# Kernel optimization log

Measured on AMD Instinct MI355X. Metric: run time of the kernel, lower is better.

Reference implementation:

```python
import jax, jax.numpy as jnp
import numpy as np

N_NODES = 50000
N_EDGES = 1600000
IN_DIM = 1024
HID = 2048
OUT = 3
BN_EPS = 1e-5


def _degree_norms(src, dst):
    ones = jnp.ones((src.shape[0],), jnp.float32)
    out_deg = jax.ops.segment_sum(ones, src, num_segments=N_NODES)
    in_deg = jax.ops.segment_sum(ones, dst, num_segments=N_NODES)
    # DGL GraphConv norm='both' clamps degrees to min 1
    out_norm = jnp.clip(out_deg, 1.0) ** -0.5
    in_norm = jnp.clip(in_deg, 1.0) ** -0.5
    return out_norm, in_norm


def _graph_conv(h, src, dst, out_norm, in_norm, W, b):
    # symmetric-normalized SpMM aggregate then dense transform (DGL GraphConv, norm='both')
    h = h * out_norm[:, None]
    msg = h[src]                                   # [E, F] gather
    agg = jax.ops.segment_sum(msg, dst, num_segments=N_NODES)
    agg = agg * in_norm[:, None]
    return agg @ W + b


def setup_inputs() -> dict:
    key = jax.random.key(0)
    k1, k2, k3, k4, k5, k6, k7 = jax.random.split(key, 7)
    in_feat = jax.random.normal(k1, (N_NODES, IN_DIM), jnp.float32)
    src = jax.random.randint(k2, (N_EDGES,), 0, N_NODES, jnp.int32)
    dst = jax.random.randint(k3, (N_EDGES,), 0, N_NODES, jnp.int32)
    W1 = jax.random.normal(k4, (IN_DIM, HID), jnp.float32) * (1.0 / np.sqrt(IN_DIM))
    b1 = jnp.zeros((HID,), jnp.float32)
    Wout = jax.random.normal(k5, (HID, OUT), jnp.float32) * (1.0 / np.sqrt(HID))
    bout = jnp.zeros((OUT,), jnp.float32)
    return {"in_feat": in_feat, "src": src, "dst": dst,
            "W1": W1, "b1": b1, "Wout": Wout, "bout": bout}


def reference(in_feat, src, dst, W1, b1, Wout, bout):
    out_norm, in_norm = _degree_norms(src, dst)
    h = _graph_conv(in_feat, src, dst, out_norm, in_norm, W1, b1)
    h = jax.nn.relu(h)
    # freshly-instantiated BatchNorm1d in training mode: batch stats, gamma=1, beta=0
    mean = jnp.mean(h, axis=0, keepdims=True)
    var = jnp.var(h, axis=0, keepdims=True)
    h = (h - mean) * jax.lax.rsqrt(var + BN_EPS)
    h = _graph_conv(h, src, dst, out_norm, in_norm, Wout, bout)
    return jax.nn.softmax(h, axis=1)
```

## Files before the change

kernel.cpp:

```cpp
#include <hip/hip_runtime.h>
#include <hip/hip_bf16.h>
#include <stdint.h>

#define N_NODES 50000
#define N_EDGES 1600000
#define IN_DIM  1024
#define HID     2048
#define OUTC    3
#define M_PAD   50048
#define BN_EPS  1e-5f

#define SCAN_CH 512
#define NCH     98

#define NPAN    32
#define PF      32
#define PSTRIDE ((size_t)M_PAD * PF)
#define NGRP    782
#define NXCD    8
#define DUMMY_SRC N_NODES
#define E_PAD_MAX (N_EDGES + 3 * N_NODES)

typedef __bf16 bf16_t;
typedef __bf16 bf16x4_t __attribute__((ext_vector_type(4)));
typedef __bf16 bf16x8_t __attribute__((ext_vector_type(8)));
typedef float  f32x4_t  __attribute__((ext_vector_type(4)));

__device__ __forceinline__ void gl2lds16(const void* g, void* l) {
  __builtin_amdgcn_global_load_lds((const __attribute__((address_space(1))) uint32_t*)g,
                                   (__attribute__((address_space(3))) uint32_t*)l,
                                   16, 0, 0);
}

__global__ void k_hist(const int* __restrict__ src, const int* __restrict__ dst,
                       int* out_cnt, int* in_cnt) {
  int e = blockIdx.x * 256 + threadIdx.x;
  if (e < N_EDGES) {
    atomicAdd(&out_cnt[src[e]], 1);
    atomicAdd(&in_cnt[dst[e]], 1);
  }
}

__global__ void k_norms(const int* __restrict__ out_cnt, const int* __restrict__ in_cnt,
                        float* out_norm, float* in_norm) {
  int i = blockIdx.x * 256 + threadIdx.x;
  if (i < N_NODES) {
    out_norm[i] = rsqrtf((float)max(out_cnt[i], 1));
    in_norm[i]  = rsqrtf((float)max(in_cnt[i], 1));
  }
}

__global__ void k_scan1(const int* __restrict__ deg, int* incl, int* partial) {
  __shared__ int s[SCAN_CH];
  int tid = threadIdx.x;
  int i = blockIdx.x * SCAN_CH + tid;
  int v = (i < N_NODES) ? ((deg[i] + 3) & ~3) : 0;
  s[tid] = v;
  for (int off = 1; off < SCAN_CH; off <<= 1) {
    __syncthreads();
    int x = (tid >= off) ? s[tid - off] : 0;
    __syncthreads();
    s[tid] += x;
  }
  __syncthreads();
  if (i < N_NODES) incl[i] = s[tid];
  if (tid == SCAN_CH - 1) partial[blockIdx.x] = s[tid];
}

__global__ void k_scan2(const int* __restrict__ partial, int* chunk_off, int* row_ptr) {
  if (threadIdx.x == 0 && blockIdx.x == 0) {
    int run = 0;
    for (int b = 0; b < NCH; b++) { chunk_off[b] = run; run += partial[b]; }
    row_ptr[N_NODES] = run;
  }
}

__global__ void k_scan3(const int* __restrict__ deg, const int* __restrict__ incl,
                        const int* __restrict__ chunk_off, int* row_ptr, int* cursor) {
  int i = blockIdx.x * SCAN_CH + threadIdx.x;
  if (i < N_NODES) {
    int dp = (deg[i] + 3) & ~3;
    int e = chunk_off[blockIdx.x] + incl[i] - dp;
    row_ptr[i] = e;
    cursor[i]  = e;
  }
}

__global__ void k_fill(const int* __restrict__ src, const int* __restrict__ dst,
                       int* cursor, int* csr_src) {
  int e = blockIdx.x * 256 + threadIdx.x;
  if (e < N_EDGES) {
    int p = atomicAdd(&cursor[dst[e]], 1);
    csr_src[p] = src[e];
  }
}

__global__ void k_pad(const int* __restrict__ in_cnt, const int* __restrict__ row_ptr,
                      int* csr_src) {
  int i = blockIdx.x * 256 + threadIdx.x;
  if (i < N_NODES) {
    int d = in_cnt[i], dp = (d + 3) & ~3;
    int base = row_ptr[i];
    for (int j = d; j < dp; j++) csr_src[base + j] = DUMMY_SRC;
  }
}

__global__ void k_conv(const float* __restrict__ in_feat, const float* __restrict__ out_norm,
                       bf16_t* __restrict__ xbp) {
  int node = blockIdx.x, t = threadIdx.x;
  int p = t >> 3, fo = (t & 7) * 4;
  bf16x4_t o;
  if (node < N_NODES) {
    float on = out_norm[node];
    float4 v = *(const float4*)(in_feat + (size_t)node * IN_DIM + p * PF + fo);
    o[0] = (bf16_t)(v.x * on); o[1] = (bf16_t)(v.y * on);
    o[2] = (bf16_t)(v.z * on); o[3] = (bf16_t)(v.w * on);
  } else {
    o[0] = (bf16_t)0.f; o[1] = (bf16_t)0.f; o[2] = (bf16_t)0.f; o[3] = (bf16_t)0.f;
  }
  *(bf16x4_t*)(xbp + (size_t)p * PSTRIDE + (size_t)node * PF + fo) = o;
}

__global__ void __launch_bounds__(256)
k_agg1(const bf16_t* __restrict__ xbp, const int* __restrict__ row_ptr,
       const int* __restrict__ csr_src, const float* __restrict__ in_norm,
       bf16_t* __restrict__ aggb) {
  int b = blockIdx.x;
  int xcd = b & (NXCD - 1), seq = b >> 3;
  int phase = seq / NGRP, grp = seq - phase * NGRP;
  int panel = xcd + (phase << 3);
  int wv = threadIdx.x >> 6, lane = threadIdx.x & 63;
  int ch = lane >> 2, seg = lane & 3;
  int node = grp * 64 + wv * 16 + ch;

  const bf16_t* xp = xbp + (size_t)panel * PSTRIDE + (seg << 3);

  int beg = 0, end = 0;
  if (node < N_NODES) { beg = row_ptr[node]; end = row_ptr[node + 1]; }

  float acc[8];
#pragma unroll
  for (int j = 0; j < 8; j++) acc[j] = 0.f;

  for (int e = beg; e < end; e += 4) {
    int my = __builtin_nontemporal_load(csr_src + e + seg);
    int i0 = __shfl(my, 0, 4);
    int i1 = __shfl(my, 1, 4);
    int i2 = __shfl(my, 2, 4);
    int i3 = __shfl(my, 3, 4);
    bf16x8_t v0 = *(const bf16x8_t*)(xp + ((size_t)(unsigned)i0 << 5));
    bf16x8_t v1 = *(const bf16x8_t*)(xp + ((size_t)(unsigned)i1 << 5));
    bf16x8_t v2 = *(const bf16x8_t*)(xp + ((size_t)(unsigned)i2 << 5));
    bf16x8_t v3 = *(const bf16x8_t*)(xp + ((size_t)(unsigned)i3 << 5));
#pragma unroll
    for (int j = 0; j < 8; j++) acc[j] += (float)v0[j];
#pragma unroll
    for (int j = 0; j < 8; j++) acc[j] += (float)v1[j];
#pragma unroll
    for (int j = 0; j < 8; j++) acc[j] += (float)v2[j];
#pragma unroll
    for (int j = 0; j < 8; j++) acc[j] += (float)v3[j];
  }

  float inn = (node < N_NODES) ? in_norm[node] : 0.f;
  bf16x8_t o;
#pragma unroll
  for (int j = 0; j < 8; j++) o[j] = (bf16_t)(acc[j] * inn);
  __builtin_nontemporal_store(o,
      (bf16x8_t*)(aggb + (size_t)node * IN_DIM + panel * PF + (seg << 3)));
}

__global__ void k_w1t(const float* __restrict__ W1, bf16_t* __restrict__ W1t) {
  __shared__ float tile[32][33];
  int k0 = blockIdx.x * 32, n0 = blockIdx.y * 32;
  int tx = threadIdx.x & 31, ty = threadIdx.x >> 5;
#pragma unroll
  for (int r = 0; r < 32; r += 8)
    tile[ty + r][tx] = W1[(size_t)(k0 + ty + r) * HID + n0 + tx];
  __syncthreads();
#pragma unroll
  for (int r = 0; r < 32; r += 8)
    W1t[(size_t)(n0 + ty + r) * IN_DIM + k0 + tx] = (bf16_t)tile[tx][ty + r];
}

__global__ void __launch_bounds__(256)
k_gemm1(const bf16_t* __restrict__ A, const bf16_t* __restrict__ Bt,
        const float* __restrict__ b1, bf16_t* __restrict__ C,
        float* __restrict__ colsum, float* __restrict__ colsq) {
  __shared__ bf16_t As[128 * 32];
  __shared__ bf16_t Bs[128 * 32];
  int t = threadIdx.x;
  const int m0 = blockIdx.y * 128, n0 = blockIdx.x * 128;

  int lrow = t >> 2, lseg = t & 3;
  const bf16_t* aG0 = A + (size_t)(m0 + lrow) * IN_DIM + lseg * 8;
  const bf16_t* aG1 = aG0 + (size_t)64 * IN_DIM;
  const bf16_t* bG0 = Bt + (size_t)(n0 + lrow) * IN_DIM + lseg * 8;
  const bf16_t* bG1 = bG0 + (size_t)64 * IN_DIM;
  bf16_t* aL0 = As + t * 8; bf16_t* aL1 = As + 2048 + t * 8;
  bf16_t* bL0 = Bs + t * 8; bf16_t* bL1 = Bs + 2048 + t * 8;

  int wv = t >> 6, ln = t & 63;
  int wm = (wv >> 1) * 64, wn = (wv & 1) * 64;
  int fr = ln & 15, fq = ln >> 4;
  const bf16_t* aF = As + (wm + fr) * 32 + fq * 8;
  const bf16_t* bF = Bs + (wn + fr) * 32 + fq * 8;

  f32x4_t acc[4][4];
#pragma unroll
  for (int i = 0; i < 4; i++)
#pragma unroll
    for (int j = 0; j < 4; j++) { acc[i][j][0]=0.f; acc[i][j][1]=0.f; acc[i][j][2]=0.f; acc[i][j][3]=0.f; }

  for (int kt = 0; kt < IN_DIM; kt += 32) {
    __syncthreads();
    gl2lds16(aG0 + kt, aL0);
    gl2lds16(aG1 + kt, aL1);
    gl2lds16(bG0 + kt, bL0);
    gl2lds16(bG1 + kt, bL1);
    __syncthreads();
    bf16x8_t af[4], bfr[4];
#pragma unroll
    for (int i = 0; i < 4; i++) af[i]  = *(const bf16x8_t*)(aF + i * 16 * 32);
#pragma unroll
    for (int j = 0; j < 4; j++) bfr[j] = *(const bf16x8_t*)(bF + j * 16 * 32);
#pragma unroll
    for (int i = 0; i < 4; i++)
#pragma unroll
      for (int j = 0; j < 4; j++)
        acc[i][j] = __builtin_amdgcn_mfma_f32_16x16x32_bf16(af[i], bfr[j], acc[i][j], 0, 0, 0);
  }

#pragma unroll
  for (int j = 0; j < 4; j++) {
    int col = n0 + wn + j * 16 + fr;
    float bias = b1[col];
    float s = 0.f, ss = 0.f;
#pragma unroll
    for (int i = 0; i < 4; i++) {
#pragma unroll
      for (int r = 0; r < 4; r++) {
        int row = m0 + wm + i * 16 + fq * 4 + r;
        float v = acc[i][j][r] + bias;
        v = v > 0.f ? v : 0.f;
        bf16_t bv = (bf16_t)v;
        __builtin_nontemporal_store(*(short*)&bv, (short*)&C[(size_t)row * HID + col]);
        if (row < N_NODES) { s += v; ss += v * v; }
      }
    }
    s  += __shfl_xor(s, 16);  s  += __shfl_xor(s, 32);
    ss += __shfl_xor(ss, 16); ss += __shfl_xor(ss, 32);
    if (fq == 0) {
      atomicAdd(&colsum[col], s);
      atomicAdd(&colsq[col], ss);
    }
  }
}

__global__ void k_bnfin(const float* __restrict__ colsum, const float* __restrict__ colsq,
                        const float* __restrict__ Wout,
                        float* cw0, float* cw1, float* cw2, float* mrs) {
  int f = blockIdx.x * 256 + threadIdx.x;
  if (f < HID) {
    float mean = colsum[f] * (1.f / N_NODES);
    float var  = colsq[f] * (1.f / N_NODES) - mean * mean;
    float rs   = rsqrtf(var + BN_EPS);
    cw0[f] = rs * Wout[f * 3 + 0];
    cw1[f] = rs * Wout[f * 3 + 1];
    cw2[f] = rs * Wout[f * 3 + 2];
    mrs[f] = mean * rs;
  }
}

__global__ void k_ct(const float* __restrict__ mrs, const float* __restrict__ Wout, float* ct) {
  __shared__ float red[3][256];
  int tid = threadIdx.x;
  float s0 = 0.f, s1 = 0.f, s2 = 0.f;
  for (int f = tid; f < HID; f += 256) {
    float m = mrs[f];
    s0 += m * Wout[f * 3 + 0];
    s1 += m * Wout[f * 3 + 1];
    s2 += m * Wout[f * 3 + 2];
  }
  red[0][tid] = s0; red[1][tid] = s1; red[2][tid] = s2;
  __syncthreads();
  for (int off = 128; off; off >>= 1) {
    if (tid < off) {
      red[0][tid] += red[0][tid + off];
      red[1][tid] += red[1][tid + off];
      red[2][tid] += red[2][tid + off];
    }
    __syncthreads();
  }
  if (tid == 0) { ct[0] = red[0][0]; ct[1] = red[1][0]; ct[2] = red[2][0]; }
}

__global__ void k_tmat(const bf16_t* __restrict__ h1, const float* __restrict__ cw0,
                       const float* __restrict__ cw1, const float* __restrict__ cw2,
                       const float* __restrict__ ct, const float* __restrict__ out_norm,
                       float4* __restrict__ t4) {
  int n = blockIdx.x, tid = threadIdx.x;
  int f0 = tid * 8;
  bf16x8_t hv = *(const bf16x8_t*)(h1 + (size_t)n * HID + f0);
  float s0 = 0.f, s1 = 0.f, s2 = 0.f;
#pragma unroll
  for (int j = 0; j < 8; j++) {
    float h = (float)hv[j];
    s0 += h * cw0[f0 + j];
    s1 += h * cw1[f0 + j];
    s2 += h * cw2[f0 + j];
  }
#pragma unroll
  for (int off = 32; off; off >>= 1) {
    s0 += __shfl_down(s0, off);
    s1 += __shfl_down(s1, off);
    s2 += __shfl_down(s2, off);
  }
  __shared__ float red[3][4];
  int wv = tid >> 6, ln = tid & 63;
  if (ln == 0) { red[0][wv] = s0; red[1][wv] = s1; red[2][wv] = s2; }
  __syncthreads();
  if (tid == 0) {
    float r0 = red[0][0] + red[0][1] + red[0][2] + red[0][3];
    float r1 = red[1][0] + red[1][1] + red[1][2] + red[1][3];
    float r2 = red[2][0] + red[2][1] + red[2][2] + red[2][3];
    float on = out_norm[n];
    t4[n] = make_float4(on * (r0 - ct[0]), on * (r1 - ct[1]), on * (r2 - ct[2]), 0.f);
  }
}

__global__ void k_out(const int* __restrict__ row_ptr, const int* __restrict__ csr_src,
                      const float4* __restrict__ t4, const float* __restrict__ in_norm,
                      const float* __restrict__ bout, float* __restrict__ out) {
  int i = blockIdx.x * 256 + threadIdx.x;
  if (i >= N_NODES) return;
  float a0 = 0.f, a1 = 0.f, a2 = 0.f;
  int beg = row_ptr[i], end = row_ptr[i + 1];
  for (int e = beg; e < end; e++) {
    float4 tv = t4[csr_src[e]];
    a0 += tv.x; a1 += tv.y; a2 += tv.z;
  }
  float inn = in_norm[i];
  float l0 = inn * a0 + bout[0];
  float l1 = inn * a1 + bout[1];
  float l2 = inn * a2 + bout[2];
  float m = fmaxf(l0, fmaxf(l1, l2));
  float e0 = expf(l0 - m), e1 = expf(l1 - m), e2 = expf(l2 - m);
  float rs = 1.f / (e0 + e1 + e2);
  out[i * 3 + 0] = e0 * rs;
  out[i * 3 + 1] = e1 * rs;
  out[i * 3 + 2] = e2 * rs;
}

extern "C" void kernel_launch(void* const* d_in, const int* in_sizes, int n_in,
                              void* d_out, int out_size, void* d_ws, size_t ws_size,
                              hipStream_t stream) {
  const float* in_feat = (const float*)d_in[0];
  const int*   src     = (const int*)d_in[1];
  const int*   dst     = (const int*)d_in[2];
  const float* W1      = (const float*)d_in[3];
  const float* b1      = (const float*)d_in[4];
  const float* Wout    = (const float*)d_in[5];
  const float* bout    = (const float*)d_in[6];
  float* out = (float*)d_out;

  char* p = (char*)d_ws;
  auto alloc = [&](size_t bytes) { char* r = p; p += (bytes + 255) & ~(size_t)255; return r; };
  bf16_t* h1      = (bf16_t*)alloc((size_t)M_PAD * HID * 2);
  bf16_t* aggb    = (bf16_t*)alloc((size_t)M_PAD * IN_DIM * 2);
  bf16_t* xbp     = (bf16_t*)alloc((size_t)NPAN * PSTRIDE * 2);
  bf16_t* W1t     = (bf16_t*)alloc((size_t)HID * IN_DIM * 2);
  int* csr_src    = (int*)alloc((size_t)E_PAD_MAX * 4);
  int* row_ptr    = (int*)alloc((size_t)(N_NODES + 1) * 4);
  int* cursor     = (int*)alloc((size_t)N_NODES * 4);
  int* incl       = (int*)alloc((size_t)N_NODES * 4);
  int* partial    = (int*)alloc((size_t)NCH * 4);
  int* chunk_off  = (int*)alloc((size_t)NCH * 4);
  int* out_cnt    = (int*)alloc((size_t)N_NODES * 4);
  int* in_cnt     = (int*)alloc((size_t)N_NODES * 4);
  float* out_norm = (float*)alloc((size_t)N_NODES * 4);
  float* in_norm  = (float*)alloc((size_t)N_NODES * 4);
  float* colsum   = (float*)alloc((size_t)HID * 4);
  float* colsq    = (float*)alloc((size_t)HID * 4);
  float* cw0      = (float*)alloc((size_t)HID * 4);
  float* cw1      = (float*)alloc((size_t)HID * 4);
  float* cw2      = (float*)alloc((size_t)HID * 4);
  float* mrs      = (float*)alloc((size_t)HID * 4);
  float* ct       = (float*)alloc(4 * 4);
  float4* t4      = (float4*)alloc((size_t)M_PAD * 16);

  hipMemsetAsync(out_cnt, 0, (size_t)N_NODES * 4, stream);
  hipMemsetAsync(in_cnt,  0, (size_t)N_NODES * 4, stream);
  hipMemsetAsync(colsum,  0, (size_t)HID * 4, stream);
  hipMemsetAsync(colsq,   0, (size_t)HID * 4, stream);
  hipMemsetAsync(t4 + N_NODES, 0, (size_t)(M_PAD - N_NODES) * 16, stream);

  k_hist <<<(N_EDGES + 255) / 256, 256, 0, stream>>>(src, dst, out_cnt, in_cnt);
  k_norms<<<(N_NODES + 255) / 256, 256, 0, stream>>>(out_cnt, in_cnt, out_norm, in_norm);
  k_conv <<<M_PAD, 256, 0, stream>>>(in_feat, out_norm, xbp);
  k_scan1<<<NCH, SCAN_CH, 0, stream>>>(in_cnt, incl, partial);
  k_scan2<<<1, 64, 0, stream>>>(partial, chunk_off, row_ptr);
  k_scan3<<<NCH, SCAN_CH, 0, stream>>>(in_cnt, incl, chunk_off, row_ptr, cursor);
  k_pad  <<<(N_NODES + 255) / 256, 256, 0, stream>>>(in_cnt, row_ptr, csr_src);
  k_fill <<<(N_EDGES + 255) / 256, 256, 0, stream>>>(src, dst, cursor, csr_src);
  k_w1t  <<<dim3(IN_DIM / 32, HID / 32), 256, 0, stream>>>(W1, W1t);
  k_agg1 <<<NXCD * (NPAN / NXCD) * NGRP, 256, 0, stream>>>(xbp, row_ptr, csr_src, in_norm, aggb);
  k_gemm1<<<dim3(HID / 128, M_PAD / 128), 256, 0, stream>>>(aggb, W1t, b1, h1, colsum, colsq);
  k_bnfin<<<HID / 256, 256, 0, stream>>>(colsum, colsq, Wout, cw0, cw1, cw2, mrs);
  k_ct   <<<1, 256, 0, stream>>>(mrs, Wout, ct);
  k_tmat <<<N_NODES, 256, 0, stream>>>(h1, cw0, cw1, cw2, ct, out_norm, t4);
  k_out  <<<(N_NODES + 255) / 256, 256, 0, stream>>>(row_ptr, csr_src, t4, in_norm, bout, out);
}
```

Baseline: 1.571 ms.

## Sort nodes by in-degree for aggregation and prefetch edge indices

Adds a counting sort of nodes by padded in-degree bucket. The aggregation kernel processes nodes in that order, so the lanes of a wave have similar edge counts and less divergence. The gather loop now reads CSR indices as 16-byte vectors, fetched two iterations ahead, and issues 8 gathers per step instead of shuffling 4 scalar loads. The cost is three extra small kernels and scattered output writes, since the perm order breaks contiguity of aggb stores.

```diff
diff --git a/kernel.cpp b/kernel.cpp
--- a/kernel.cpp
+++ b/kernel.cpp
@@ -19,17 +19,27 @@
 #define NGRP    782
 #define NXCD    8
 #define DUMMY_SRC N_NODES
-#define E_PAD_MAX (N_EDGES + 3 * N_NODES)
+#define E_PAD_MAX (N_EDGES + 3 * N_NODES + 64)
+#define DBINS   256
 
 typedef __bf16 bf16_t;
 typedef __bf16 bf16x4_t __attribute__((ext_vector_type(4)));
 typedef __bf16 bf16x8_t __attribute__((ext_vector_type(8)));
 typedef float  f32x4_t  __attribute__((ext_vector_type(4)));
+typedef int    i32x4_t  __attribute__((ext_vector_type(4)));
 
 __device__ __forceinline__ void gl2lds16(const void* g, void* l) {
   __builtin_amdgcn_global_load_lds((const __attribute__((address_space(1))) uint32_t*)g,
                                    (__attribute__((address_space(3))) uint32_t*)l,
                                    16, 0, 0);
+}
+
+__device__ __forceinline__ i32x4_t nt4(const int* p) {
+  return __builtin_nontemporal_load((const i32x4_t*)p);
+}
+
+__device__ __forceinline__ bf16x8_t gat(const bf16_t* xp, int i) {
+  return *(const bf16x8_t*)(xp + ((size_t)(unsigned)i << 5));
 }
 
 __global__ void k_hist(const int* __restrict__ src, const int* __restrict__ dst,
@@ -47,6 +57,29 @@
   if (i < N_NODES) {
     out_norm[i] = rsqrtf((float)max(out_cnt[i], 1));
     in_norm[i]  = rsqrtf((float)max(in_cnt[i], 1));
+  }
+}
+
+__global__ void k_dhist(const int* __restrict__ in_cnt, int* dhist) {
+  int i = blockIdx.x * 256 + threadIdx.x;
+  if (i < N_NODES) {
+    int b = min((in_cnt[i] + 3) >> 2, DBINS - 1);
+    atomicAdd(&dhist[b], 1);
+  }
+}
+
+__global__ void k_dscan(const int* __restrict__ dhist, int* doff, int* dcur) {
+  if (threadIdx.x == 0 && blockIdx.x == 0) {
+    int run = 0;
+    for (int b = 0; b < DBINS; b++) { doff[b] = run; dcur[b] = run; run += dhist[b]; }
+  }
+}
+
+__global__ void k_dscat(const int* __restrict__ in_cnt, int* dcur, int* perm) {
+  int i = blockIdx.x * 256 + threadIdx.x;
+  if (i < N_NODES) {
+    int b = min((in_cnt[i] + 3) >> 2, DBINS - 1);
+    perm[atomicAdd(&dcur[b], 1)] = i;
   }
 }
 
@@ -124,14 +157,15 @@
 __global__ void __launch_bounds__(256)
 k_agg1(const bf16_t* __restrict__ xbp, const int* __restrict__ row_ptr,
        const int* __restrict__ csr_src, const float* __restrict__ in_norm,
-       bf16_t* __restrict__ aggb) {
+       const int* __restrict__ perm, bf16_t* __restrict__ aggb) {
   int b = blockIdx.x;
   int xcd = b & (NXCD - 1), seq = b >> 3;
   int phase = seq / NGRP, grp = seq - phase * NGRP;
   int panel = xcd + (phase << 3);
   int wv = threadIdx.x >> 6, lane = threadIdx.x & 63;
   int ch = lane >> 2, seg = lane & 3;
-  int node = grp * 64 + wv * 16 + ch;
+  int idx = grp * 64 + wv * 16 + ch;
+  int node = (idx < N_NODES) ? perm[idx] : N_NODES;
 
   const bf16_t* xp = xbp + (size_t)panel * PSTRIDE + (seg << 3);
 
@@ -142,16 +176,58 @@
 #pragma unroll
   for (int j = 0; j < 8; j++) acc[j] = 0.f;
 
-  for (int e = beg; e < end; e += 4) {
-    int my = __builtin_nontemporal_load(csr_src + e + seg);
-    int i0 = __shfl(my, 0, 4);
-    int i1 = __shfl(my, 1, 4);
-    int i2 = __shfl(my, 2, 4);
-    int i3 = __shfl(my, 3, 4);
-    bf16x8_t v0 = *(const bf16x8_t*)(xp + ((size_t)(unsigned)i0 << 5));
-    bf16x8_t v1 = *(const bf16x8_t*)(xp + ((size_t)(unsigned)i1 << 5));
-    bf16x8_t v2 = *(const bf16x8_t*)(xp + ((size_t)(unsigned)i2 << 5));
-    bf16x8_t v3 = *(const bf16x8_t*)(xp + ((size_t)(unsigned)i3 << 5));
+  int e = beg;
+  i32x4_t a0, b0, a1, b1;
+  if (e + 8 <= end)  { a0 = nt4(csr_src + e);     b0 = nt4(csr_src + e + 4); }
+  if (e + 16 <= end) { a1 = nt4(csr_src + e + 8); b1 = nt4(csr_src + e + 12); }
+
+  for (; e + 16 <= end; e += 8) {
+    bf16x8_t v0 = gat(xp, a0.x), v1 = gat(xp, a0.y), v2 = gat(xp, a0.z), v3 = gat(xp, a0.w);
+    bf16x8_t v4 = gat(xp, b0.x), v5 = gat(xp, b0.y), v6 = gat(xp, b0.z), v7 = gat(xp, b0.w);
+    a0 = a1; b0 = b1;
+    a1 = nt4(csr_src + e + 16);
+    b1 = nt4(csr_src + e + 20);
+#pragma unroll
+    for (int j = 0; j < 8; j++) acc[j] += (float)v0[j];
+#pragma unroll
+    for (int j = 0; j < 8; j++) acc[j] += (float)v1[j];
+#pragma unroll
+    for (int j = 0; j < 8; j++) acc[j] += (float)v2[j];
+#pragma unroll
+    for (int j = 0; j < 8; j++) acc[j] += (float)v3[j];
+#pragma unroll
+    for (int j = 0; j < 8; j++) acc[j] += (float)v4[j];
+#pragma unroll
+    for (int j = 0; j < 8; j++) acc[j] += (float)v5[j];
+#pragma unroll
+    for (int j = 0; j < 8; j++) acc[j] += (float)v6[j];
+#pragma unroll
+    for (int j = 0; j < 8; j++) acc[j] += (float)v7[j];
+  }
+  if (e + 8 <= end) {
+    bf16x8_t v0 = gat(xp, a0.x), v1 = gat(xp, a0.y), v2 = gat(xp, a0.z), v3 = gat(xp, a0.w);
+    bf16x8_t v4 = gat(xp, b0.x), v5 = gat(xp, b0.y), v6 = gat(xp, b0.z), v7 = gat(xp, b0.w);
+#pragma unroll
+    for (int j = 0; j < 8; j++) acc[j] += (float)v0[j];
+#pragma unroll
+    for (int j = 0; j < 8; j++) acc[j] += (float)v1[j];
+#pragma unroll
+    for (int j = 0; j < 8; j++) acc[j] += (float)v2[j];
+#pragma unroll
+    for (int j = 0; j < 8; j++) acc[j] += (float)v3[j];
+#pragma unroll
+    for (int j = 0; j < 8; j++) acc[j] += (float)v4[j];
+#pragma unroll
+    for (int j = 0; j < 8; j++) acc[j] += (float)v5[j];
+#pragma unroll
+    for (int j = 0; j < 8; j++) acc[j] += (float)v6[j];
+#pragma unroll
+    for (int j = 0; j < 8; j++) acc[j] += (float)v7[j];
+    e += 8;
+  }
+  if (e + 4 <= end) {
+    i32x4_t c = nt4(csr_src + e);
+    bf16x8_t v0 = gat(xp, c.x), v1 = gat(xp, c.y), v2 = gat(xp, c.z), v3 = gat(xp, c.w);
 #pragma unroll
     for (int j = 0; j < 8; j++) acc[j] += (float)v0[j];
 #pragma unroll
@@ -378,6 +454,10 @@
   int* chunk_off  = (int*)alloc((size_t)NCH * 4);
   int* out_cnt    = (int*)alloc((size_t)N_NODES * 4);
   int* in_cnt     = (int*)alloc((size_t)N_NODES * 4);
+  int* perm       = (int*)alloc((size_t)N_NODES * 4);
+  int* dhist      = (int*)alloc((size_t)DBINS * 4);
+  int* doff       = (int*)alloc((size_t)DBINS * 4);
+  int* dcur       = (int*)alloc((size_t)DBINS * 4);
   float* out_norm = (float*)alloc((size_t)N_NODES * 4);
   float* in_norm  = (float*)alloc((size_t)N_NODES * 4);
   float* colsum   = (float*)alloc((size_t)HID * 4);
@@ -391,6 +471,7 @@
 
   hipMemsetAsync(out_cnt, 0, (size_t)N_NODES * 4, stream);
   hipMemsetAsync(in_cnt,  0, (size_t)N_NODES * 4, stream);
+  hipMemsetAsync(dhist,   0, (size_t)DBINS * 4, stream);
   hipMemsetAsync(colsum,  0, (size_t)HID * 4, stream);
   hipMemsetAsync(colsq,   0, (size_t)HID * 4, stream);
   hipMemsetAsync(t4 + N_NODES, 0, (size_t)(M_PAD - N_NODES) * 16, stream);
@@ -398,13 +479,16 @@
   k_hist <<<(N_EDGES + 255) / 256, 256, 0, stream>>>(src, dst, out_cnt, in_cnt);
   k_norms<<<(N_NODES + 255) / 256, 256, 0, stream>>>(out_cnt, in_cnt, out_norm, in_norm);
   k_conv <<<M_PAD, 256, 0, stream>>>(in_feat, out_norm, xbp);
+  k_dhist<<<(N_NODES + 255) / 256, 256, 0, stream>>>(in_cnt, dhist);
+  k_dscan<<<1, 64, 0, stream>>>(dhist, doff, dcur);
+  k_dscat<<<(N_NODES + 255) / 256, 256, 0, stream>>>(in_cnt, dcur, perm);
   k_scan1<<<NCH, SCAN_CH, 0, stream>>>(in_cnt, incl, partial);
   k_scan2<<<1, 64, 0, stream>>>(partial, chunk_off, row_ptr);
   k_scan3<<<NCH, SCAN_CH, 0, stream>>>(in_cnt, incl, chunk_off, row_ptr, cursor);
   k_pad  <<<(N_NODES + 255) / 256, 256, 0, stream>>>(in_cnt, row_ptr, csr_src);
   k_fill <<<(N_EDGES + 255) / 256, 256, 0, stream>>>(src, dst, cursor, csr_src);
   k_w1t  <<<dim3(IN_DIM / 32, HID / 32), 256, 0, stream>>>(W1, W1t);
-  k_agg1 <<<NXCD * (NPAN / NXCD) * NGRP, 256, 0, stream>>>(xbp, row_ptr, csr_src, in_norm, aggb);
+  k_agg1 <<<NXCD * (NPAN / NXCD) * NGRP, 256, 0, stream>>>(xbp, row_ptr, csr_src, in_norm, perm, aggb);
   k_gemm1<<<dim3(HID / 128, M_PAD / 128), 256, 0, stream>>>(aggb, W1t, b1, h1, colsum, colsq);
   k_bnfin<<<HID / 256, 256, 0, stream>>>(colsum, colsq, Wout, cw0, cw1, cw2, mrs);
   k_ct   <<<1, 256, 0, stream>>>(mrs, Wout, ct);
```

Result: slower. 2.039 ms (+29.8%).

## Widen feature panels and assign one wavefront per node in aggregation

Applied to the files above, without the earlier changes.

The bf16 feature panels grow from 32 to 64 features, so there are 16 panels, and the first-layer aggregation now gives each destination node a full wavefront. Eight lane groups each gather a different neighbor's 128-byte row, and the partial sums are combined with cross-lane xor shuffles. The aim is more memory-level parallelism per node and fewer panel passes over the CSR index list. In exchange the grid gets much larger, shuffle reductions are added, and tail edges need masking. Wasted lanes on low-degree nodes are also possible.

```diff
diff --git a/kernel.cpp b/kernel.cpp
--- a/kernel.cpp
+++ b/kernel.cpp
@@ -13,13 +13,13 @@
 #define SCAN_CH 512
 #define NCH     98
 
-#define NPAN    32
-#define PF      32
+#define NPAN    16
+#define PF      64
 #define PSTRIDE ((size_t)M_PAD * PF)
-#define NGRP    782
+#define NGRP4   12512
 #define NXCD    8
 #define DUMMY_SRC N_NODES
-#define E_PAD_MAX (N_EDGES + 3 * N_NODES)
+#define E_PAD_MAX (N_EDGES + 3 * N_NODES + 64)
 
 typedef __bf16 bf16_t;
 typedef __bf16 bf16x4_t __attribute__((ext_vector_type(4)));
@@ -108,7 +108,7 @@
 __global__ void k_conv(const float* __restrict__ in_feat, const float* __restrict__ out_norm,
                        bf16_t* __restrict__ xbp) {
   int node = blockIdx.x, t = threadIdx.x;
-  int p = t >> 3, fo = (t & 7) * 4;
+  int p = t >> 4, fo = (t & 15) * 4;
   bf16x4_t o;
   if (node < N_NODES) {
     float on = out_norm[node];
@@ -127,13 +127,13 @@
        bf16_t* __restrict__ aggb) {
   int b = blockIdx.x;
   int xcd = b & (NXCD - 1), seq = b >> 3;
-  int phase = seq / NGRP, grp = seq - phase * NGRP;
+  int phase = seq / NGRP4, grp = seq - phase * NGRP4;
   int panel = xcd + (phase << 3);
   int wv = threadIdx.x >> 6, lane = threadIdx.x & 63;
-  int ch = lane >> 2, seg = lane & 3;
-  int node = grp * 64 + wv * 16 + ch;
-
-  const bf16_t* xp = xbp + (size_t)panel * PSTRIDE + (seg << 3);
+  int sub = lane >> 3, fo = (lane & 7) << 3;
+  int node = grp * 4 + wv;
+
+  const bf16_t* xp = xbp + (size_t)panel * PSTRIDE + fo;
 
   int beg = 0, end = 0;
   if (node < N_NODES) { beg = row_ptr[node]; end = row_ptr[node + 1]; }
@@ -142,32 +142,46 @@
 #pragma unroll
   for (int j = 0; j < 8; j++) acc[j] = 0.f;
 
-  for (int e = beg; e < end; e += 4) {
-    int my = __builtin_nontemporal_load(csr_src + e + seg);
-    int i0 = __shfl(my, 0, 4);
-    int i1 = __shfl(my, 1, 4);
-    int i2 = __shfl(my, 2, 4);
-    int i3 = __shfl(my, 3, 4);
-    bf16x8_t v0 = *(const bf16x8_t*)(xp + ((size_t)(unsigned)i0 << 5));
-    bf16x8_t v1 = *(const bf16x8_t*)(xp + ((size_t)(unsigned)i1 << 5));
-    bf16x8_t v2 = *(const bf16x8_t*)(xp + ((size_t)(unsigned)i2 << 5));
-    bf16x8_t v3 = *(const bf16x8_t*)(xp + ((size_t)(unsigned)i3 << 5));
+  int e = beg;
+  for (; e + 16 <= end; e += 16) {
+    int s0 = __builtin_nontemporal_load(csr_src + e + sub);
+    int s1 = __builtin_nontemporal_load(csr_src + e + 8 + sub);
+    bf16x8_t v0 = *(const bf16x8_t*)(xp + ((size_t)(unsigned)s0 << 6));
+    bf16x8_t v1 = *(const bf16x8_t*)(xp + ((size_t)(unsigned)s1 << 6));
 #pragma unroll
     for (int j = 0; j < 8; j++) acc[j] += (float)v0[j];
 #pragma unroll
     for (int j = 0; j < 8; j++) acc[j] += (float)v1[j];
-#pragma unroll
-    for (int j = 0; j < 8; j++) acc[j] += (float)v2[j];
-#pragma unroll
-    for (int j = 0; j < 8; j++) acc[j] += (float)v3[j];
-  }
-
-  float inn = (node < N_NODES) ? in_norm[node] : 0.f;
-  bf16x8_t o;
-#pragma unroll
-  for (int j = 0; j < 8; j++) o[j] = (bf16_t)(acc[j] * inn);
-  __builtin_nontemporal_store(o,
-      (bf16x8_t*)(aggb + (size_t)node * IN_DIM + panel * PF + (seg << 3)));
+  }
+  if (e + 8 <= end) {
+    int s0 = __builtin_nontemporal_load(csr_src + e + sub);
+    bf16x8_t v0 = *(const bf16x8_t*)(xp + ((size_t)(unsigned)s0 << 6));
+#pragma unroll
+    for (int j = 0; j < 8; j++) acc[j] += (float)v0[j];
+    e += 8;
+  }
+  if (e < end && sub < 4) {
+    int s0 = __builtin_nontemporal_load(csr_src + e + sub);
+    bf16x8_t v0 = *(const bf16x8_t*)(xp + ((size_t)(unsigned)s0 << 6));
+#pragma unroll
+    for (int j = 0; j < 8; j++) acc[j] += (float)v0[j];
+  }
+
+#pragma unroll
+  for (int j = 0; j < 8; j++) {
+    acc[j] += __shfl_xor(acc[j], 8);
+    acc[j] += __shfl_xor(acc[j], 16);
+    acc[j] += __shfl_xor(acc[j], 32);
+  }
+
+  if (sub == 0) {
+    float inn = (node < N_NODES) ? in_norm[node] : 0.f;
+    bf16x8_t o;
+#pragma unroll
+    for (int j = 0; j < 8; j++) o[j] = (bf16_t)(acc[j] * inn);
+    __builtin_nontemporal_store(o,
+        (bf16x8_t*)(aggb + (size_t)node * IN_DIM + panel * PF + fo));
+  }
 }
 
 __global__ void k_w1t(const float* __restrict__ W1, bf16_t* __restrict__ W1t) {
@@ -404,7 +418,7 @@
   k_pad  <<<(N_NODES + 255) / 256, 256, 0, stream>>>(in_cnt, row_ptr, csr_src);
   k_fill <<<(N_EDGES + 255) / 256, 256, 0, stream>>>(src, dst, cursor, csr_src);
   k_w1t  <<<dim3(IN_DIM / 32, HID / 32), 256, 0, stream>>>(W1, W1t);
-  k_agg1 <<<NXCD * (NPAN / NXCD) * NGRP, 256, 0, stream>>>(xbp, row_ptr, csr_src, in_norm, aggb);
+  k_agg1 <<<NXCD * (NPAN / NXCD) * NGRP4, 256, 0, stream>>>(xbp, row_ptr, csr_src, in_norm, aggb);
   k_gemm1<<<dim3(HID / 128, M_PAD / 128), 256, 0, stream>>>(aggb, W1t, b1, h1, colsum, colsq);
   k_bnfin<<<HID / 256, 256, 0, stream>>>(colsum, colsq, Wout, cw0, cw1, cw2, mrs);
   k_ct   <<<1, 256, 0, stream>>>(mrs, Wout, ct);
```

Result: faster. 1.491 ms (-5.1%).
